# Kernel tuning notes

Measured on AMD Instinct MI355X. Metric: run time of the kernel, lower is better.

## Reference

```python
import jax, jax.numpy as jnp
import numpy as np

# Geometry constants (from init_kwargs geo)
VIEWS = 512
NDET = 736
NX = 256
NY = 256
EXTENT = 2
CHANNEL = 1
START_ANGLE = 0.0
END_ANGLE = 2.0 * np.pi
SCALE = (END_ANGLE - START_ANGLE) / (2.0 * VIEWS * EXTENT)
SINO_LEN = VIEWS * NDET            # 376832
IDX_LEN = NX * NY * VIEWS * EXTENT  # 67108864


def setup_inputs() -> dict:
    key = jax.random.key(0)
    k1, k2, k3, k4 = jax.random.split(key, 4)
    x = jax.random.normal(k1, (1, CHANNEL, SINO_LEN), dtype=jnp.float32)
    weight = jax.random.uniform(k2, (IDX_LEN,), dtype=jnp.float32)
    bias = jax.random.normal(k3, (NX * NY,), dtype=jnp.float32)
    indices = jax.random.randint(k4, (IDX_LEN,), 0, SINO_LEN, dtype=jnp.int64)
    return {"x": x, "weight": weight, "bias": bias, "indices": indices}


def reference(x, weight, bias, indices):
    # x: [B, C, views*nDetecU]
    sino = x.reshape(-1, CHANNEL, SINO_LEN)
    # Irregular gather: [B, C, NX*NY*views*extent]
    g = jnp.take(sino, indices, axis=2)
    # Learned per-ray weighting (DotProduct)
    g = g * weight  # broadcast over leading [B, C]
    # Group by voxel, sum over views*extent, scale by angular step
    g = g.reshape(-1, CHANNEL, NX * NY, VIEWS * EXTENT)
    out = jnp.sum(g, axis=3) * jnp.float32(SCALE)
    out = out + bias  # broadcast over [B, C]
    out = out.reshape(-1, CHANNEL, NX, NY)
    out = jnp.flip(out, axis=(2, 3))
    return out
```

## Files before the change

### kernel.cpp

```cpp
#include <hip/hip_runtime.h>
#include <math.h>
#include <stdint.h>

#define VIEWS 512
#define NDET 736
#define NX 256
#define NY 256
#define EXTENT 2
#define SINO_LEN (VIEWS * NDET)
#define NVOX (NX * NY)
#define PER_VOX (VIEWS * EXTENT)

__device__ __constant__ float kScale = (float)(M_PI / 1024.0);

typedef int   v4i __attribute__((ext_vector_type(4)));
typedef float v4f __attribute__((ext_vector_type(4)));

__global__ __launch_bounds__(256) void backproj_kernel(
    const float* __restrict__ x,
    const float* __restrict__ weight,
    const float* __restrict__ bias,
    const int*   __restrict__ indices,
    float*       __restrict__ out)
{
    const int wave_in_block = threadIdx.x >> 6;
    const int lane          = threadIdx.x & 63;
    const int v             = blockIdx.x * 4 + wave_in_block;
    const size_t base       = (size_t)v * PER_VOX;

    const v4i* ip = (const v4i*)(indices + base);
    const v4f* wp = (const v4f*)(weight + base);

    v4i i4[4];
#pragma unroll
    for (int k = 0; k < 4; ++k)
        i4[k] = __builtin_nontemporal_load(&ip[lane + k * 64]);

    float g[16];
#pragma unroll
    for (int k = 0; k < 4; ++k) {
        g[4 * k + 0] = x[i4[k].x];
        g[4 * k + 1] = x[i4[k].y];
        g[4 * k + 2] = x[i4[k].z];
        g[4 * k + 3] = x[i4[k].w];
    }

    v4f w4[4];
#pragma unroll
    for (int k = 0; k < 4; ++k)
        w4[k] = __builtin_nontemporal_load(&wp[lane + k * 64]);

    float s = 0.0f;
#pragma unroll
    for (int k = 0; k < 4; ++k) {
        s += g[4 * k + 0] * w4[k].x;
        s += g[4 * k + 1] * w4[k].y;
        s += g[4 * k + 2] * w4[k].z;
        s += g[4 * k + 3] * w4[k].w;
    }

#pragma unroll
    for (int off = 32; off > 0; off >>= 1)
        s += __shfl_down(s, off, 64);

    if (lane == 0) {
        out[NVOX - 1 - v] = bias[v] + kScale * s;
    }
}

extern "C" void kernel_launch(void* const* d_in, const int* in_sizes, int n_in,
                              void* d_out, int out_size, void* d_ws, size_t ws_size,
                              hipStream_t stream) {
    const float* x       = (const float*)d_in[0];
    const float* weight  = (const float*)d_in[1];
    const float* bias    = (const float*)d_in[2];
    const int*   indices = (const int*)d_in[3];
    float*       out     = (float*)d_out;

    const int blocks = NVOX / 4;
    backproj_kernel<<<blocks, 256, 0, stream>>>(x, weight, bias, indices, out);
}
```

Measured before the change: 683.9 us.

## Stage fp16 sinogram segments in LDS and gather from shared memory

Converts the sinogram to fp16 in a workspace, then each block streams it through a 64KB LDS buffer over 12 passes, using async global-to-LDS loads. Each thread gathers only the indices that fall into the current segment, masking out the rest. This replaces random global/L2 gathers with LDS reads, at the cost of reduced precision for x, repeated full-sinogram streaming per block, and twelve masked LDS passes per index.

```diff
diff --git a/kernel.cpp b/kernel.cpp
--- a/kernel.cpp
+++ b/kernel.cpp
@@ -1,4 +1,5 @@
 #include <hip/hip_runtime.h>
+#include <hip/hip_fp16.h>
 #include <math.h>
 #include <stdint.h>
 
@@ -11,12 +12,129 @@
 #define NVOX (NX * NY)
 #define PER_VOX (VIEWS * EXTENT)
 
+#define SEGB 65536
+#define NPASS 12
+#define XWS_BYTES (NPASS * SEGB)
+#define XWS_HALVES (XWS_BYTES / 2)
+
 __device__ __constant__ float kScale = (float)(M_PI / 1024.0);
 
 typedef int   v4i __attribute__((ext_vector_type(4)));
 typedef float v4f __attribute__((ext_vector_type(4)));
 
-__global__ __launch_bounds__(256) void backproj_kernel(
+__global__ __launch_bounds__(256) void convert_x_kernel(
+    const float* __restrict__ x, ushort* __restrict__ xh)
+{
+    const int t = blockIdx.x * 256 + threadIdx.x;
+    const int e = t * 4;
+    ushort4 u;
+    if (e < SINO_LEN) {
+        const float4 v = *(const float4*)(x + e);
+        u.x = __half_as_ushort(__float2half(v.x));
+        u.y = __half_as_ushort(__float2half(v.y));
+        u.z = __half_as_ushort(__float2half(v.z));
+        u.w = __half_as_ushort(__float2half(v.w));
+    } else {
+        u.x = u.y = u.z = u.w = 0;
+    }
+    *(ushort4*)(xh + e) = u;
+}
+
+__global__ __launch_bounds__(512, 4) void backproj_lds_kernel(
+    const ushort* __restrict__ xh,
+    const float*  __restrict__ weight,
+    const float*  __restrict__ bias,
+    const int*    __restrict__ indices,
+    float*        __restrict__ out)
+{
+    extern __shared__ unsigned char xs[];
+
+    const int tid  = threadIdx.x;
+    const int lane = tid & 63;
+    const int wid  = tid >> 6;
+    const int vv   = tid >> 5;
+    const int q    = tid & 31;
+
+    const int    vox0  = blockIdx.x * 16;
+    const size_t pbase = (size_t)(vox0 + vv) * PER_VOX;
+
+    const v4i* ip = (const v4i*)(indices + pbase);
+    const v4f* wp = (const v4f*)(weight + pbase);
+
+    v4i i4[8];
+    v4f w4[8];
+#pragma unroll
+    for (int k = 0; k < 8; ++k) i4[k] = __builtin_nontemporal_load(&ip[q + k * 32]);
+#pragma unroll
+    for (int k = 0; k < 8; ++k) w4[k] = __builtin_nontemporal_load(&wp[q + k * 32]);
+#pragma unroll
+    for (int k = 0; k < 8; ++k) {
+        i4[k].x <<= 1; i4[k].y <<= 1; i4[k].z <<= 1; i4[k].w <<= 1;
+    }
+
+    const unsigned sbase = (unsigned)(wid * 8192 + lane * 16);
+
+    float s = 0.0f;
+
+    for (int p = 0; p < NPASS; ++p) {
+        const unsigned loB = (unsigned)p * SEGB;
+
+#pragma unroll
+        for (int k = 0; k < 8; ++k) {
+            const unsigned off = sbase + (unsigned)(k * 1024);
+            __builtin_amdgcn_global_load_lds(
+                (const __attribute__((address_space(1))) unsigned int*)
+                    ((const unsigned char*)xh + loB + off),
+                (__attribute__((address_space(3))) unsigned int*)(xs + off),
+                16, 0, 0);
+        }
+        __syncthreads();
+
+#pragma unroll
+        for (int k = 0; k < 8; ++k) {
+            {
+                const unsigned off = (unsigned)i4[k].x - loB;
+                const bool in = off < (unsigned)SEGB;
+                const unsigned a = in ? off : 0u;
+                const float val = __half2float(*(const __half*)(xs + a));
+                s = fmaf(val, in ? w4[k].x : 0.0f, s);
+            }
+            {
+                const unsigned off = (unsigned)i4[k].y - loB;
+                const bool in = off < (unsigned)SEGB;
+                const unsigned a = in ? off : 0u;
+                const float val = __half2float(*(const __half*)(xs + a));
+                s = fmaf(val, in ? w4[k].y : 0.0f, s);
+            }
+            {
+                const unsigned off = (unsigned)i4[k].z - loB;
+                const bool in = off < (unsigned)SEGB;
+                const unsigned a = in ? off : 0u;
+                const float val = __half2float(*(const __half*)(xs + a));
+                s = fmaf(val, in ? w4[k].z : 0.0f, s);
+            }
+            {
+                const unsigned off = (unsigned)i4[k].w - loB;
+                const bool in = off < (unsigned)SEGB;
+                const unsigned a = in ? off : 0u;
+                const float val = __half2float(*(const __half*)(xs + a));
+                s = fmaf(val, in ? w4[k].w : 0.0f, s);
+            }
+        }
+        __syncthreads();
+    }
+
+#pragma unroll
+    for (int off = 16; off > 0; off >>= 1)
+        s += __shfl_xor(s, off, 64);
+
+    if (q == 0) {
+        const int v = vox0 + vv;
+        out[NVOX - 1 - v] = bias[v] + kScale * s;
+    }
+}
+
+__global__ __launch_bounds__(256) void backproj_fallback_kernel(
     const float* __restrict__ x,
     const float* __restrict__ weight,
     const float* __restrict__ bias,
@@ -63,9 +181,8 @@
     for (int off = 32; off > 0; off >>= 1)
         s += __shfl_down(s, off, 64);
 
-    if (lane == 0) {
+    if (lane == 0)
         out[NVOX - 1 - v] = bias[v] + kScale * s;
-    }
 }
 
 extern "C" void kernel_launch(void* const* d_in, const int* in_sizes, int n_in,
@@ -77,6 +194,13 @@
     const int*   indices = (const int*)d_in[3];
     float*       out     = (float*)d_out;
 
-    const int blocks = NVOX / 4;
-    backproj_kernel<<<blocks, 256, 0, stream>>>(x, weight, bias, indices, out);
-}
+    if (ws_size >= (size_t)XWS_BYTES) {
+        ushort* xh = (ushort*)d_ws;
+        convert_x_kernel<<<XWS_HALVES / 4 / 256, 256, 0, stream>>>(x, xh);
+        backproj_lds_kernel<<<NVOX / 16, 512, SEGB, stream>>>(
+            xh, weight, bias, indices, out);
+    } else {
+        backproj_fallback_kernel<<<NVOX / 4, 256, 0, stream>>>(
+            x, weight, bias, indices, out);
+    }
+}
```

Result: faster. 613.1 us (-10.4%).
